# Performance work log

Hardware: AMD Instinct MI355X
Metric: run time of the kernel (lower is better)

The kernel has to match this reference:

```python
import jax, jax.numpy as jnp
import numpy as np
from jax import lax

# ---- static module constants (the torch module's registered buffers) ----
NRB = 8            # num_radial_basis
RAD = 2.5          # diameter / 2
GRID = 192         # voxel grid extent
N = 200000         # occupied voxels
DIM = 80           # 32x0e + 16x1o
ALPHA = 1.0 / np.sqrt(48.0)   # e3nn path normalization (fan_in = 32 + 16 into each output irrep)

_ax = np.arange(-2.0, 3.0, dtype=np.float32)                        # floor(2.5/1.0)=2 -> 5 taps/axis
LATTICE = np.stack(np.meshgrid(_ax, _ax, _ax, indexing='ij'), -1)   # [5,5,5,3]
PERM = np.arange(125).reshape(5, 5, 5).transpose(2, 1, 0).reshape(-1)  # einsum('xyz...->zyx...') as a flat permutation
OFFS = LATTICE.reshape(-1, 3).astype(np.int32)[PERM]                # voxel offsets, ordered to match permuted kernel


def _radial_emb():
    # soft_one_hot_linspace(..., basis='smooth_finite', cutoff=True)
    d = np.linalg.norm(LATTICE, axis=-1)
    centers = np.linspace(0.0, RAD, NRB + 2)[1:-1]
    step = centers[1] - centers[0]
    t = (d[..., None] - centers) / step
    inside = np.abs(t) < 1.0
    safe = np.where(inside, 1.0 - t * t, 1.0)
    return (1.14136 * np.exp(2.0) * np.where(inside, np.exp(-2.0 / safe), 0.0)).astype(np.float32)

EMB = _radial_emb().reshape(-1, NRB)  # [125, 8]


def _sph():
    # spherical harmonics l=0,1; normalize=True, normalization='component' (|Y_l|^2 = 2l+1)
    n = np.linalg.norm(LATTICE, axis=-1, keepdims=True)
    u = np.where(n > 0, LATTICE / np.maximum(n, 1e-9), 0.0)
    return np.concatenate([np.ones_like(n), np.sqrt(3.0) * u], -1).astype(np.float32)

SH = _sph().reshape(-1, 4)  # [125, 4]


def make_kernel(weight):
    # kernel(): (emb @ weight) / numel(lattice), then tp.right(sh, w) -> [tap, dim_in, dim_out]
    w = jnp.asarray(EMB) @ weight / 125.0        # [125, 2304]
    w1 = w[:, :1024].reshape(125, 32, 32)        # path 0e x 0e -> 0e
    w2 = w[:, 1024:1536].reshape(125, 32, 16)    # path 0e x 1o -> 1o
    w3 = w[:, 1536:1792].reshape(125, 16, 16)    # path 1o x 0e -> 1o
    w4 = w[:, 1792:].reshape(125, 16, 32)        # path 1o x 1o -> 0e (dot product)
    s0 = jnp.asarray(SH[:, 0])
    v = jnp.asarray(SH[:, 1:])
    eye3 = jnp.eye(3, dtype=w.dtype)
    K00 = ALPHA * w1 * s0[:, None, None]                                                  # [125,32,32]
    K01 = ALPHA * jnp.einsum('pik,pm->pikm', w2, v).reshape(125, 32, 48)                  # [125,32,48]
    K11 = ALPHA * jnp.einsum('pik,mn->pimkn', w3 * s0[:, None, None], eye3).reshape(125, 48, 48)
    K10 = (ALPHA / np.sqrt(3.0)) * jnp.einsum('pik,pm->pimk', w4, v).reshape(125, 48, 32)
    K = jnp.concatenate([jnp.concatenate([K00, K01], 2), jnp.concatenate([K10, K11], 2)], 1)
    return K[jnp.asarray(PERM)]  # xyz -> zyx tap order + flatten


def _forward(feats, weight, w_sc0, w_sc1, coords):
    kern = make_kernel(weight)  # [125, 80, 80]
    # residual e3nn Linear: per-irrep channel mixing with 1/sqrt(fan_in) normalization
    sc0 = feats[:, :32] @ (w_sc0 / np.sqrt(32.0))
    sc1 = jnp.einsum('nim,ik->nkm', feats[:, 32:].reshape(-1, 16, 3), w_sc1 / np.sqrt(16.0)).reshape(-1, 48)
    sc = jnp.concatenate([sc0, sc1], -1)
    # Minkowski sparse voxel conv: dense index volume -> per-tap gather / GEMM / accumulate
    n = coords.shape[0]
    idx_vol = jnp.full((GRID, GRID, GRID), -1, jnp.int32)
    idx_vol = idx_vol.at[coords[:, 0], coords[:, 1], coords[:, 2]].set(jnp.arange(n, dtype=jnp.int32))

    def tap(acc, oK):
        off, Ko = oK
        c = coords + off                                  # [N,3] neighbor coords for this tap
        ok = jnp.all((c >= 0) & (c < GRID), axis=1)
        cc = jnp.clip(c, 0, GRID - 1)
        nb = idx_vol[cc[:, 0], cc[:, 1], cc[:, 2]]        # [N] row index or -1
        f = jnp.where((ok & (nb >= 0))[:, None], feats[jnp.maximum(nb, 0)], 0.0)
        return acc + f @ Ko, None

    out, _ = lax.scan(tap, jnp.zeros(feats.shape, feats.dtype), (jnp.asarray(OFFS), kern))
    return sc + out


def setup_inputs() -> dict:
    key = jax.random.key(0)
    k1, k2, k3, k4 = jax.random.split(key, 4)
    rng = np.random.default_rng(0)
    lin = rng.choice(GRID ** 3, size=N, replace=False)  # unique occupied voxels
    coords = np.stack([lin // (GRID * GRID), (lin // GRID) % GRID, lin % GRID], 1).astype(np.int32)
    return {
        'feats': jax.random.normal(k1, (N, DIM), jnp.float32),
        'weight': jax.random.normal(k2, (NRB, 2304), jnp.float32),
        'w_sc0': jax.random.normal(k3, (32, 32), jnp.float32),
        'w_sc1': jax.random.normal(k4, (16, 16), jnp.float32),
        'coords': jnp.asarray(coords),
    }


def reference(feats, weight, w_sc0, w_sc1, coords):
    return _forward(feats, weight, w_sc0, w_sc1, coords)
```

## Files before the change

### kernel.cpp

```cpp
#include <hip/hip_runtime.h>

#define N_PTS 200000
#define GRIDL 192
#define CAP 8192
#define NREG 216
#define RCAP 1152
#define NSLICE 9
#define SCAP 32

#define VOL_OFF   0ull
#define VOL_BYTES (192ull*192ull*192ull*4ull)
#define BINS_OFF  28311552ull
#define BCNT_OFF  36503552ull
#define RCNT_OFF  36519552ull
#define PLIST_OFF 36547200ull
#define WBUF_OFF  38537856ull
#define VTAB_OFF  39689856ull
#define A0_OFF    39691856ull
#define A1_OFF    39695952ull

struct TapTable { int p[80]; };
__host__ __device__ constexpr TapTable make_taps() {
    TapTable tt{}; int t = 0;
    for (int a = -2; a <= 2; a++)
        for (int b = -2; b <= 2; b++)
            for (int c = -2; c <= 2; c++) {
                int sq = a*a + b*b + c*c;
                if (sq >= 1 && sq <= 6) tt.p[t++] = (a+2)*25 + (b+2)*5 + (c+2);
            }
    return tt;
}
__device__ const TapTable TAPS = make_taps();

__global__ void prep_kernel(const float* __restrict__ wt, const float* __restrict__ wsc0,
                            const float* __restrict__ wsc1, float* __restrict__ wbuf,
                            float* __restrict__ vtab, float* __restrict__ A0,
                            float* __restrict__ A1) {
    int p = blockIdx.x;
    int dx = p / 25 - 2, dy = (p / 5) % 5 - 2, dz = p % 5 - 2;
    double d = sqrt((double)(dx*dx + dy*dy + dz*dz));
    const double step = 2.5 / 9.0;
    const double cst = 1.14136 * exp(2.0);
    float emb[8];
#pragma unroll
    for (int r = 0; r < 8; r++) {
        double t = (d - (double)(r + 1) * step) / step;
        double tt = t * t;
        emb[r] = (tt < 1.0) ? (float)(cst * exp(-2.0 / (1.0 - tt))) : 0.0f;
    }
    if (threadIdx.x == 0) {
        float inv = (d > 0.0) ? (float)(sqrt(3.0) / d) : 0.0f;
        vtab[p*4+0] = dx * inv; vtab[p*4+1] = dy * inv;
        vtab[p*4+2] = dz * inv; vtab[p*4+3] = 0.0f;
    }
    const float ALPHA = 0.14433756729740643f;
    for (int q = threadIdx.x; q < 2304; q += blockDim.x) {
        float acc = 0.0f;
#pragma unroll
        for (int r = 0; r < 8; r++) acc = fmaf(emb[r], wt[r*2304 + q], acc);
        acc *= (1.0f / 125.0f);
        float val = acc * ((q < 1792) ? ALPHA : (1.0f / 12.0f));
        wbuf[p*2304 + q] = val;
        if (p == 62) {
            if (q < 1024)                   A0[q]        = wsc0[q] * 0.17677669529663687f + val;
            else if (q >= 1536 && q < 1792) A1[q-1536]   = wsc1[q-1536] * 0.25f + val;
        }
    }
}

__global__ __launch_bounds__(256) void scatter_kernel(const int* __restrict__ coords,
        int* __restrict__ vol, int* __restrict__ rcnt_pad, int2* __restrict__ plist) {
    __shared__ int hist[216];
    __shared__ int rbase[216];
    for (int i = threadIdx.x; i < 216; i += 256) hist[i] = 0;
    __syncthreads();
    for (int n = blockIdx.x * 256 + threadIdx.x; n < N_PTS; n += 65536) {
        int x = coords[n*3], y = coords[n*3+1], z = coords[n*3+2];
        vol[(x * GRIDL + y) * GRIDL + z] = n;
        int r = (x >> 5) * 36 + (y >> 5) * 6 + (z >> 5);
        atomicAdd(&hist[r], 1);
    }
    __syncthreads();
    if (threadIdx.x < 216) {
        int c = hist[threadIdx.x];
        rbase[threadIdx.x] = c ? atomicAdd(&rcnt_pad[threadIdx.x * 32], c) : 0;
        hist[threadIdx.x] = 0;
    }
    __syncthreads();
    for (int n = blockIdx.x * 256 + threadIdx.x; n < N_PTS; n += 65536) {
        int x = coords[n*3], y = coords[n*3+1], z = coords[n*3+2];
        int r = (x >> 5) * 36 + (y >> 5) * 6 + (z >> 5);
        int j = rbase[r] + atomicAdd(&hist[r], 1);
        if (j < RCAP) plist[r * RCAP + j] = make_int2(n, (x << 16) | (y << 8) | z);
    }
}

__global__ __launch_bounds__(128) void enum_kernel(const int* __restrict__ vol,
        const int* __restrict__ rcnt_pad, const int2* __restrict__ plist,
        int* __restrict__ bcnt_pad, int2* __restrict__ bins) {
    int r = blockIdx.x / NSLICE, s = blockIdx.x % NSLICE;
    int cnt = min(rcnt_pad[r * 32], RCAP);
    int lo = s * 128, hi = min(cnt, lo + 128);
    if (lo >= hi) return;
    __shared__ int2 stage[80][SCAP];
    __shared__ int hist[80];
    __shared__ int tbase[80];
    if (threadIdx.x < 80) hist[threadIdx.x] = 0;
    __syncthreads();

    int idx = lo + threadIdx.x;
    bool act = idx < hi;
    int n = -1, x = 0, y = 0, z = 0;
    if (act) {
        int2 e = plist[r * RCAP + idx];
        n = e.x; x = e.y >> 16; y = (e.y >> 8) & 255; z = e.y & 255;
    }
    int t = 0;
#pragma unroll
    for (int a = -2; a <= 2; a++)
#pragma unroll
    for (int b = -2; b <= 2; b++)
#pragma unroll
    for (int c = -2; c <= 2; c++) {
        int sq = a*a + b*b + c*c;
        if (sq < 1 || sq > 6) continue;
        int cx = x + a, cy = y + b, cz = z + c;
        if (act && ((unsigned)cx < 192u) && ((unsigned)cy < 192u) && ((unsigned)cz < 192u)) {
            int nb = vol[(cx * GRIDL + cy) * GRIDL + cz];
            if (nb >= 0) {
                int j = atomicAdd(&hist[t], 1);
                if (j < SCAP) stage[t][j] = make_int2(n, nb);
            }
        }
        t++;
    }
    __syncthreads();
    if (threadIdx.x < 80) {
        int c = min(hist[threadIdx.x], SCAP);
        tbase[threadIdx.x] = c ? atomicAdd(&bcnt_pad[TAPS.p[threadIdx.x] * 32], c) : 0;
    }
    __syncthreads();
    int g = threadIdx.x >> 5, l = threadIdx.x & 31;
    for (int q = 0; q < 20; q++) {
        int t2 = g * 20 + q;
        int c = min(hist[t2], SCAP);
        if (l < c) {
            int pos = tbase[t2] + l;
            if (pos < CAP) bins[TAPS.p[t2] * CAP + pos] = stage[t2][l];
        }
    }
}

__global__ __launch_bounds__(256) void sc_self_kernel(const float* __restrict__ feats,
        const float* __restrict__ A0, const float* __restrict__ A1,
        float* __restrict__ out) {
    __shared__ __align__(16) float sA0[1024];
    __shared__ __align__(16) float sA1[256];
    for (int i = threadIdx.x; i < 1024; i += 256) sA0[i] = A0[i];
    if (threadIdx.x < 256) sA1[threadIdx.x] = A1[threadIdx.x];
    __syncthreads();
    int n = blockIdx.x * 256 + threadIdx.x;
    if (n >= N_PTS) return;
    const float4* fr = (const float4*)(feats + (size_t)n * 80);
    float4* orow = (float4*)(out + (size_t)n * 80);
    float f0[32];
#pragma unroll
    for (int j = 0; j < 8; j++) {
        float4 t = fr[j];
        f0[4*j] = t.x; f0[4*j+1] = t.y; f0[4*j+2] = t.z; f0[4*j+3] = t.w;
    }
    float a0[32];
#pragma unroll
    for (int k = 0; k < 32; k++) a0[k] = 0.0f;
#pragma unroll
    for (int i = 0; i < 32; i++) {
        float fv = f0[i];
#pragma unroll
        for (int k4 = 0; k4 < 8; k4++) {
            float4 w = ((const float4*)sA0)[i*8 + k4];
            a0[4*k4]   = fmaf(fv, w.x, a0[4*k4]);
            a0[4*k4+1] = fmaf(fv, w.y, a0[4*k4+1]);
            a0[4*k4+2] = fmaf(fv, w.z, a0[4*k4+2]);
            a0[4*k4+3] = fmaf(fv, w.w, a0[4*k4+3]);
        }
    }
#pragma unroll
    for (int j = 0; j < 8; j++) orow[j] = make_float4(a0[4*j], a0[4*j+1], a0[4*j+2], a0[4*j+3]);
    float f1[48];
#pragma unroll
    for (int j = 0; j < 12; j++) {
        float4 t = fr[8 + j];
        f1[4*j] = t.x; f1[4*j+1] = t.y; f1[4*j+2] = t.z; f1[4*j+3] = t.w;
    }
    float a1[48];
#pragma unroll
    for (int k = 0; k < 48; k++) a1[k] = 0.0f;
#pragma unroll
    for (int i = 0; i < 16; i++) {
        float fm0 = f1[3*i], fm1 = f1[3*i+1], fm2 = f1[3*i+2];
#pragma unroll
        for (int k4 = 0; k4 < 4; k4++) {
            float4 w = ((const float4*)sA1)[i*4 + k4];
            const float* wp = (const float*)&w;
#pragma unroll
            for (int kk = 0; kk < 4; kk++) {
                int k = 4*k4 + kk;
                a1[3*k]   = fmaf(fm0, wp[kk], a1[3*k]);
                a1[3*k+1] = fmaf(fm1, wp[kk], a1[3*k+1]);
                a1[3*k+2] = fmaf(fm2, wp[kk], a1[3*k+2]);
            }
        }
    }
#pragma unroll
    for (int j = 0; j < 12; j++) orow[8+j] = make_float4(a1[4*j], a1[4*j+1], a1[4*j+2], a1[4*j+3]);
}

__global__ __launch_bounds__(256) void bin_kernel(const float* __restrict__ feats,
        const float* __restrict__ wbuf, const float* __restrict__ vtab,
        const int* __restrict__ bcnt_pad, const int2* __restrict__ bins,
        float* __restrict__ out) {
    int p = blockIdx.x >> 3;
    int chunk = blockIdx.x & 7;
    int cnt = min(bcnt_pad[p * 32], CAP);
    int start = chunk * 1024;
    if (start >= cnt) return;

    __shared__ __align__(16) float sW[2304];
    __shared__ float sv[4];
    __shared__ __align__(16) float ys[4][16][81];

    for (int i = threadIdx.x; i < 2304; i += 256) sW[i] = wbuf[p*2304 + i];
    if (threadIdx.x < 4) sv[threadIdx.x] = vtab[p*4 + threadIdx.x];
    __syncthreads();

    int wv = threadIdx.x >> 6, lane = threadIdx.x & 63;
    const float4* sW1 = (const float4*)sW;
    const float4* sW2 = (const float4*)(sW + 1024);
    const float4* sW3 = (const float4*)(sW + 1536);
    const float4* sW4 = (const float4*)(sW + 1792);
    float v0 = sv[0], v1 = sv[1], v2 = sv[2];

    for (int it = 0; it < 4; it++) {
        int h = start + wv * 256 + it * 64 + lane;
        bool act = h < cnt;
        int n = -1, nb = 0;
        if (act) { int2 e = bins[p*CAP + h]; n = e.x; nb = e.y; }

        const float4* fr = (const float4*)(feats + (size_t)nb * 80);
        float f0[32], f1[48];
#pragma unroll
        for (int j = 0; j < 8; j++) {
            float4 t = fr[j];
            f0[4*j] = t.x; f0[4*j+1] = t.y; f0[4*j+2] = t.z; f0[4*j+3] = t.w;
        }
#pragma unroll
        for (int j = 0; j < 12; j++) {
            float4 t = fr[8 + j];
            f1[4*j] = t.x; f1[4*j+1] = t.y; f1[4*j+2] = t.z; f1[4*j+3] = t.w;
        }
        float g[16];
#pragma unroll
        for (int i = 0; i < 16; i++)
            g[i] = f1[3*i]*v0 + f1[3*i+1]*v1 + f1[3*i+2]*v2;

        float a0[32], cc[16];
#pragma unroll
        for (int k = 0; k < 32; k++) a0[k] = 0.0f;
#pragma unroll
        for (int k = 0; k < 16; k++) cc[k] = 0.0f;
#pragma unroll
        for (int i = 0; i < 32; i++) {
            float fv = f0[i];
#pragma unroll
            for (int k4 = 0; k4 < 8; k4++) {
                float4 w = sW1[i*8 + k4];
                a0[4*k4]   = fmaf(fv, w.x, a0[4*k4]);
                a0[4*k4+1] = fmaf(fv, w.y, a0[4*k4+1]);
                a0[4*k4+2] = fmaf(fv, w.z, a0[4*k4+2]);
                a0[4*k4+3] = fmaf(fv, w.w, a0[4*k4+3]);
            }
#pragma unroll
            for (int k4 = 0; k4 < 4; k4++) {
                float4 w = sW2[i*4 + k4];
                cc[4*k4]   = fmaf(fv, w.x, cc[4*k4]);
                cc[4*k4+1] = fmaf(fv, w.y, cc[4*k4+1]);
                cc[4*k4+2] = fmaf(fv, w.z, cc[4*k4+2]);
                cc[4*k4+3] = fmaf(fv, w.w, cc[4*k4+3]);
            }
        }
#pragma unroll
        for (int i = 0; i < 16; i++) {
            float gv = g[i];
#pragma unroll
            for (int k4 = 0; k4 < 8; k4++) {
                float4 w = sW4[i*8 + k4];
                a0[4*k4]   = fmaf(gv, w.x, a0[4*k4]);
                a0[4*k4+1] = fmaf(gv, w.y, a0[4*k4+1]);
                a0[4*k4+2] = fmaf(gv, w.z, a0[4*k4+2]);
                a0[4*k4+3] = fmaf(gv, w.w, a0[4*k4+3]);
            }
        }
        float a1[48];
#pragma unroll
        for (int k = 0; k < 16; k++) {
            a1[3*k] = v0 * cc[k]; a1[3*k+1] = v1 * cc[k]; a1[3*k+2] = v2 * cc[k];
        }
#pragma unroll
        for (int i = 0; i < 16; i++) {
            float fm0 = f1[3*i], fm1 = f1[3*i+1], fm2 = f1[3*i+2];
#pragma unroll
            for (int k4 = 0; k4 < 4; k4++) {
                float4 w = sW3[i*4 + k4];
                const float* wp = (const float*)&w;
#pragma unroll
                for (int kk = 0; kk < 4; kk++) {
                    int k = 4*k4 + kk;
                    a1[3*k]   = fmaf(fm0, wp[kk], a1[3*k]);
                    a1[3*k+1] = fmaf(fm1, wp[kk], a1[3*k+1]);
                    a1[3*k+2] = fmaf(fm2, wp[kk], a1[3*k+2]);
                }
            }
        }

#pragma unroll
        for (int ph = 0; ph < 4; ph++) {
            if ((lane >> 4) == ph) {
                int rr = lane & 15;
                float* yr = &ys[wv][rr][0];
#pragma unroll
                for (int k = 0; k < 32; k++) yr[k] = a0[k];
#pragma unroll
                for (int k = 0; k < 48; k++) yr[32 + k] = a1[k];
            }
            for (int h2 = 0; h2 < 16; h2++) {
                int nn = __shfl(n, ph * 16 + h2, 64);
                if (nn < 0) continue;
                float* orow = out + (size_t)nn * 80;
                unsafeAtomicAdd(orow + lane, ys[wv][h2][lane]);
                if (lane < 16) unsafeAtomicAdd(orow + 64 + lane, ys[wv][h2][64 + lane]);
            }
        }
    }
}

extern "C" void kernel_launch(void* const* d_in, const int* in_sizes, int n_in,
                              void* d_out, int out_size, void* d_ws, size_t ws_size,
                              hipStream_t stream) {
    const float* feats = (const float*)d_in[0];
    const float* wt    = (const float*)d_in[1];
    const float* wsc0  = (const float*)d_in[2];
    const float* wsc1  = (const float*)d_in[3];
    const int*   coords= (const int*)d_in[4];
    float* out = (float*)d_out;
    char* ws = (char*)d_ws;

    int*   vol      = (int*)(ws + VOL_OFF);
    int2*  bins     = (int2*)(ws + BINS_OFF);
    int*   bcnt_pad = (int*)(ws + BCNT_OFF);
    int*   rcnt_pad = (int*)(ws + RCNT_OFF);
    int2*  plist    = (int2*)(ws + PLIST_OFF);
    float* wbuf     = (float*)(ws + WBUF_OFF);
    float* vtab     = (float*)(ws + VTAB_OFF);
    float* A0       = (float*)(ws + A0_OFF);
    float* A1       = (float*)(ws + A1_OFF);

    hipMemsetAsync(vol, 0xFF, VOL_BYTES, stream);
    hipMemsetAsync(bcnt_pad, 0, 16000 + 27648, stream);

    prep_kernel<<<125, 256, 0, stream>>>(wt, wsc0, wsc1, wbuf, vtab, A0, A1);
    scatter_kernel<<<256, 256, 0, stream>>>(coords, vol, rcnt_pad, plist);
    enum_kernel<<<NREG * NSLICE, 128, 0, stream>>>(vol, rcnt_pad, plist, bcnt_pad, bins);
    sc_self_kernel<<<(N_PTS + 255) / 256, 256, 0, stream>>>(feats, A0, A1, out);
    bin_kernel<<<125 * 8, 256, 0, stream>>>(feats, wbuf, vtab, bcnt_pad, bins, out);
}
```

Measured before the change: 516.4 us.

## Prefetch next gather in bin kernel with single-wave blocks; vectorize volume row reads

The bin kernel moves to 64-thread blocks, each handling up to 512 pairs. It software-pipelines the feature-row gather, loading the next row into registers while the current one is being computed, and drops the __syncthreads. The enum kernel now reads five consecutive volume entries as one int4 plus one scalar, instead of 80 scattered loads. The workspace is shifted by 256 bytes so the unaligned int4 read at z-2 stays inside the allocation. The cost is higher register pressure from two 20-float4 buffers, which may hurt occupancy, and possibly misaligned int4 loads.

```diff
diff --git a/kernel.cpp b/kernel.cpp
--- a/kernel.cpp
+++ b/kernel.cpp
@@ -8,16 +8,16 @@
 #define NSLICE 9
 #define SCAP 32
 
-#define VOL_OFF   0ull
+#define VOL_OFF   256ull
 #define VOL_BYTES (192ull*192ull*192ull*4ull)
-#define BINS_OFF  28311552ull
-#define BCNT_OFF  36503552ull
-#define RCNT_OFF  36519552ull
-#define PLIST_OFF 36547200ull
-#define WBUF_OFF  38537856ull
-#define VTAB_OFF  39689856ull
-#define A0_OFF    39691856ull
-#define A1_OFF    39695952ull
+#define BINS_OFF  28312064ull
+#define BCNT_OFF  36504064ull
+#define RCNT_OFF  36520064ull
+#define PLIST_OFF 36547712ull
+#define WBUF_OFF  38538368ull
+#define VTAB_OFF  39690368ull
+#define A0_OFF    39692368ull
+#define A1_OFF    39696464ull
 
 struct TapTable { int p[80]; };
 __host__ __device__ constexpr TapTable make_taps() {
@@ -117,22 +117,32 @@
     }
     int t = 0;
 #pragma unroll
-    for (int a = -2; a <= 2; a++)
-#pragma unroll
-    for (int b = -2; b <= 2; b++)
-#pragma unroll
-    for (int c = -2; c <= 2; c++) {
-        int sq = a*a + b*b + c*c;
-        if (sq < 1 || sq > 6) continue;
-        int cx = x + a, cy = y + b, cz = z + c;
-        if (act && ((unsigned)cx < 192u) && ((unsigned)cy < 192u) && ((unsigned)cz < 192u)) {
-            int nb = vol[(cx * GRIDL + cy) * GRIDL + cz];
-            if (nb >= 0) {
-                int j = atomicAdd(&hist[t], 1);
-                if (j < SCAP) stage[t][j] = make_int2(n, nb);
-            }
-        }
-        t++;
+    for (int a = -2; a <= 2; a++) {
+        int cx = x + a;
+#pragma unroll
+        for (int b = -2; b <= 2; b++) {
+            int cy = y + b;
+            bool okrow = act && ((unsigned)cx < 192u) && ((unsigned)cy < 192u);
+            int4 v4 = make_int4(-1, -1, -1, -1);
+            int v5 = -1;
+            if (okrow) {
+                const int* rowp = vol + ((cx * GRIDL + cy) * GRIDL + z);
+                v4 = *reinterpret_cast<const int4*>(rowp - 2);
+                v5 = rowp[2];
+            }
+#pragma unroll
+            for (int c = -2; c <= 2; c++) {
+                int sq = a*a + b*b + c*c;
+                if (sq < 1 || sq > 6) continue;
+                int nb = (c == -2) ? v4.x : (c == -1) ? v4.y :
+                         (c ==  0) ? v4.z : (c ==  1) ? v4.w : v5;
+                if (okrow && ((unsigned)(z + c) < 192u) && nb >= 0) {
+                    int j = atomicAdd(&hist[t], 1);
+                    if (j < SCAP) stage[t][j] = make_int2(n, nb);
+                }
+                t++;
+            }
+        }
     }
     __syncthreads();
     if (threadIdx.x < 80) {
@@ -215,48 +225,66 @@
     for (int j = 0; j < 12; j++) orow[8+j] = make_float4(a1[4*j], a1[4*j+1], a1[4*j+2], a1[4*j+3]);
 }
 
-__global__ __launch_bounds__(256) void bin_kernel(const float* __restrict__ feats,
+__global__ __launch_bounds__(64, 2) void bin_kernel(const float* __restrict__ feats,
         const float* __restrict__ wbuf, const float* __restrict__ vtab,
         const int* __restrict__ bcnt_pad, const int2* __restrict__ bins,
         float* __restrict__ out) {
-    int p = blockIdx.x >> 3;
-    int chunk = blockIdx.x & 7;
+    int p = blockIdx.x >> 4;
+    int chunk = blockIdx.x & 15;
     int cnt = min(bcnt_pad[p * 32], CAP);
-    int start = chunk * 1024;
+    int start = chunk * 512;
     if (start >= cnt) return;
 
     __shared__ __align__(16) float sW[2304];
-    __shared__ float sv[4];
-    __shared__ __align__(16) float ys[4][16][81];
-
-    for (int i = threadIdx.x; i < 2304; i += 256) sW[i] = wbuf[p*2304 + i];
-    if (threadIdx.x < 4) sv[threadIdx.x] = vtab[p*4 + threadIdx.x];
-    __syncthreads();
-
-    int wv = threadIdx.x >> 6, lane = threadIdx.x & 63;
+    __shared__ __align__(16) float ys[16][81];
+
+    int lane = threadIdx.x;
+    {
+        const float4* src = (const float4*)(wbuf + p*2304);
+        float4* dstp = (float4*)sW;
+#pragma unroll
+        for (int j = 0; j < 9; j++) dstp[j*64 + lane] = src[j*64 + lane];
+    }
+    float v0 = vtab[p*4+0], v1 = vtab[p*4+1], v2 = vtab[p*4+2];
+
     const float4* sW1 = (const float4*)sW;
     const float4* sW2 = (const float4*)(sW + 1024);
     const float4* sW3 = (const float4*)(sW + 1536);
     const float4* sW4 = (const float4*)(sW + 1792);
-    float v0 = sv[0], v1 = sv[1], v2 = sv[2];
-
-    for (int it = 0; it < 4; it++) {
-        int h = start + wv * 256 + it * 64 + lane;
-        bool act = h < cnt;
-        int n = -1, nb = 0;
-        if (act) { int2 e = bins[p*CAP + h]; n = e.x; nb = e.y; }
-
-        const float4* fr = (const float4*)(feats + (size_t)nb * 80);
+
+    int nIter = (min(cnt - start, 512) + 63) >> 6;
+
+    int h0 = start + lane;
+    int2 e_cur = (h0 < cnt) ? bins[p*CAP + h0] : make_int2(-1, 0);
+    float4 fc[20];
+    {
+        const float4* fr = (const float4*)(feats + (size_t)e_cur.y * 80);
+#pragma unroll
+        for (int j = 0; j < 20; j++) fc[j] = fr[j];
+    }
+    int h1 = h0 + 64;
+    int2 e_nxt = (h1 < cnt) ? bins[p*CAP + h1] : make_int2(-1, 0);
+
+    for (int it = 0; it < nIter; it++) {
+        float4 fn[20];
+        {
+            const float4* fr = (const float4*)(feats + (size_t)e_nxt.y * 80);
+#pragma unroll
+            for (int j = 0; j < 20; j++) fn[j] = fr[j];
+        }
+        int h2 = start + (it + 2) * 64 + lane;
+        int2 e_n2 = (h2 < cnt) ? bins[p*CAP + h2] : make_int2(-1, 0);
+
+        int n = e_cur.x;
+
         float f0[32], f1[48];
 #pragma unroll
         for (int j = 0; j < 8; j++) {
-            float4 t = fr[j];
-            f0[4*j] = t.x; f0[4*j+1] = t.y; f0[4*j+2] = t.z; f0[4*j+3] = t.w;
+            f0[4*j] = fc[j].x; f0[4*j+1] = fc[j].y; f0[4*j+2] = fc[j].z; f0[4*j+3] = fc[j].w;
         }
 #pragma unroll
         for (int j = 0; j < 12; j++) {
-            float4 t = fr[8 + j];
-            f1[4*j] = t.x; f1[4*j+1] = t.y; f1[4*j+2] = t.z; f1[4*j+3] = t.w;
+            f1[4*j] = fc[8+j].x; f1[4*j+1] = fc[8+j].y; f1[4*j+2] = fc[8+j].z; f1[4*j+3] = fc[8+j].w;
         }
         float g[16];
 #pragma unroll
@@ -326,20 +354,24 @@
         for (int ph = 0; ph < 4; ph++) {
             if ((lane >> 4) == ph) {
                 int rr = lane & 15;
-                float* yr = &ys[wv][rr][0];
+                float* yr = &ys[rr][0];
 #pragma unroll
                 for (int k = 0; k < 32; k++) yr[k] = a0[k];
 #pragma unroll
                 for (int k = 0; k < 48; k++) yr[32 + k] = a1[k];
             }
-            for (int h2 = 0; h2 < 16; h2++) {
-                int nn = __shfl(n, ph * 16 + h2, 64);
+            for (int h3 = 0; h3 < 16; h3++) {
+                int nn = __shfl(n, ph * 16 + h3, 64);
                 if (nn < 0) continue;
                 float* orow = out + (size_t)nn * 80;
-                unsafeAtomicAdd(orow + lane, ys[wv][h2][lane]);
-                if (lane < 16) unsafeAtomicAdd(orow + 64 + lane, ys[wv][h2][64 + lane]);
-            }
-        }
+                unsafeAtomicAdd(orow + lane, ys[h3][lane]);
+                if (lane < 16) unsafeAtomicAdd(orow + 64 + lane, ys[h3][64 + lane]);
+            }
+        }
+
+        e_cur = e_nxt; e_nxt = e_n2;
+#pragma unroll
+        for (int j = 0; j < 20; j++) fc[j] = fn[j];
     }
 }
 
@@ -371,5 +403,5 @@
     scatter_kernel<<<256, 256, 0, stream>>>(coords, vol, rcnt_pad, plist);
     enum_kernel<<<NREG * NSLICE, 128, 0, stream>>>(vol, rcnt_pad, plist, bcnt_pad, bins);
     sc_self_kernel<<<(N_PTS + 255) / 256, 256, 0, stream>>>(feats, A0, A1, out);
-    bin_kernel<<<125 * 8, 256, 0, stream>>>(feats, wbuf, vtab, bcnt_pad, bins, out);
-}
+    bin_kernel<<<125 * 16, 64, 0, stream>>>(feats, wbuf, vtab, bcnt_pad, bins, out);
+}
```

After: 487.5 us. 1.06x faster.
